# Optimization experiments

Measured on AMD Instinct MI355X. Metric: run time of the kernel, lower is better.

The kernel has to match this reference:

```python
import jax, jax.numpy as jnp
import numpy as np

E = 1024   # embedding_size
K = 64     # key_size
DH = 64    # head_size
H = 16     # layer_size (num heads)
F = 4096   # hidden_size
B, S = 4, 2048
EPS = float(np.finfo(np.float32).eps)  # torch RMSNorm default eps


def setup_inputs() -> dict:
    key = jax.random.key(0)
    ks = jax.random.split(key, 12)
    embeddings = jax.random.normal(ks[0], (B, S, E), dtype=jnp.float32)
    # causal additive mask: 0 on/below diagonal, -1e9 above
    tri = jnp.triu(jnp.ones((S, S), dtype=bool), k=1)
    causal_buffer = jnp.where(tri, -1e9, 0.0).astype(jnp.float32)[None]  # [1,S,S]
    # standard RoPE cos/sin buffers over the key dim
    inv_freq = 1.0 / (10000.0 ** (jnp.arange(0, K // 2, dtype=jnp.float32) * 2.0 / K))
    ang = jnp.arange(S, dtype=jnp.float32)[:, None] * inv_freq[None, :]  # [S,K/2]
    ang = jnp.concatenate([ang, ang], axis=-1)                           # [S,K]
    cos_buffer = jnp.cos(ang)[None]  # [1,S,K]
    sin_buffer = jnp.sin(ang)[None]
    sc = 0.02
    wq = jax.random.normal(ks[1], (H, E, K), dtype=jnp.float32) * sc
    wk = jax.random.normal(ks[2], (H, E, K), dtype=jnp.float32) * sc
    wv = jax.random.normal(ks[3], (H, E, DH), dtype=jnp.float32) * sc
    w_proj = jax.random.normal(ks[4], (E, E), dtype=jnp.float32) * sc
    attn_norm_w = jnp.ones((E,), dtype=jnp.float32)
    mlp_norm_w = jnp.ones((E,), dtype=jnp.float32)
    w_up = jax.random.normal(ks[5], (E, F), dtype=jnp.float32) * sc
    w_gate = jax.random.normal(ks[6], (E, F), dtype=jnp.float32) * sc
    w_down = jax.random.normal(ks[7], (F, E), dtype=jnp.float32) * sc
    return {"embeddings": embeddings, "causal_buffer": causal_buffer,
            "cos_buffer": cos_buffer, "sin_buffer": sin_buffer,
            "wq": wq, "wk": wk, "wv": wv, "w_proj": w_proj,
            "attn_norm_w": attn_norm_w, "mlp_norm_w": mlp_norm_w,
            "w_up": w_up, "w_gate": w_gate, "w_down": w_down}


def _rmsnorm(x, w):
    ms = jnp.mean(x * x, axis=-1, keepdims=True)
    return x * jax.lax.rsqrt(ms + EPS) * w


def _rotate(x, cos, sin):
    # x: [B,H,S,K]; cos/sin: [1,1,S,K]. swapped = cat(second_half, first_half)
    swapped = jnp.concatenate([x[..., K // 2:], x[..., :K // 2]], axis=-1)
    return cos * x + sin * swapped


def reference(embeddings, causal_buffer, cos_buffer, sin_buffer,
              wq, wk, wv, w_proj, attn_norm_w, mlp_norm_w,
              w_up, w_gate, w_down):
    cos = cos_buffer[:, None]  # [1,1,S,K]
    sin = sin_buffer[:, None]
    # NOTE: original computes attention_norm(embeddings) but feeds RAW
    # embeddings to the heads; we reproduce that faithfully.
    q = _rotate(jnp.einsum('bse,hek->bhsk', embeddings, wq), cos, sin)
    k = _rotate(jnp.einsum('bse,hek->bhsk', embeddings, wk), cos, sin)
    v = jnp.einsum('bse,hed->bhsd', embeddings, wv)
    scores = jnp.einsum('bhsk,bhtk->bhst', q, k) / jnp.sqrt(jnp.float32(K))
    scores = scores + causal_buffer[:, None]  # broadcast over heads
    weights = jax.nn.softmax(scores, axis=-1)
    attn = jnp.einsum('bhst,bhtd->bhsd', weights, v)  # [B,H,S,DH]
    attn = attn.transpose(0, 2, 1, 3).reshape(attn.shape[0], attn.shape[2], H * DH)
    x = embeddings + attn @ w_proj
    h = _rmsnorm(x, mlp_norm_w)
    mlp = (h @ w_up) * jax.nn.elu(h @ w_gate)
    return x + mlp @ w_down
```

## Files before the change

kernel.cpp:

```cpp
#include <hip/hip_runtime.h>
#include <cstdint>
#include <cstddef>

#define E_DIM 1024
#define S_LEN 2048
#define NB 4
#define NH 16
#define F_DIM 4096

typedef __attribute__((ext_vector_type(8))) __bf16 bf16x8;
typedef __attribute__((ext_vector_type(4))) __bf16 bf16x4;
typedef __attribute__((ext_vector_type(4))) float f32x4;
typedef __attribute__((ext_vector_type(16))) float f32x16;

__device__ __forceinline__ f32x4 mfma16(bf16x8 a, bf16x8 b, f32x4 c) {
  return __builtin_amdgcn_mfma_f32_16x16x32_bf16(a, b, c, 0, 0, 0);
}
__device__ __forceinline__ f32x16 mfma32(bf16x8 a, bf16x8 b, f32x16 c) {
  return __builtin_amdgcn_mfma_f32_32x32x16_bf16(a, b, c, 0, 0, 0);
}

__device__ __forceinline__ unsigned short f2bf(float f) {
  __bf16 h = (__bf16)f;
  return __builtin_bit_cast(unsigned short, h);
}

__device__ __forceinline__ void gl_lds16(const void* gptr, void* lptr) {
  __builtin_amdgcn_global_load_lds(
      (const __attribute__((address_space(1))) void*)gptr,
      (__attribute__((address_space(3))) void*)lptr, 16, 0, 0);
}


__global__ __launch_bounds__(256) void cast_emb_kernel(
    const float4* __restrict__ in, ushort4* __restrict__ out) {
  int i = blockIdx.x * 256 + threadIdx.x;
  float4 v = in[i];
  ushort4 o;
  o.x = f2bf(v.x); o.y = f2bf(v.y); o.z = f2bf(v.z); o.w = f2bf(v.w);
  out[i] = o;
}

__global__ __launch_bounds__(256) void transpose_cast_kernel(
    const float* __restrict__ in, unsigned short* __restrict__ out, int R, int C) {
  __shared__ float tile[32][33];
  const int bz = blockIdx.z;
  const float* ip = in + (size_t)bz * R * C;
  const int r0 = blockIdx.y * 32, c0 = blockIdx.x * 32;
  const int tc = threadIdx.x & 31, tr = threadIdx.x >> 5;
#pragma unroll
  for (int i = 0; i < 4; ++i)
    tile[tr + i * 8][tc] = ip[(size_t)(r0 + tr + i * 8) * C + (c0 + tc)];
  __syncthreads();
#pragma unroll
  for (int i = 0; i < 4; ++i)
    out[(size_t)(bz * C + c0 + tr + i * 8) * R + (r0 + tc)] = f2bf(tile[tc][tr + i * 8]);
}

__global__ __launch_bounds__(256) void transpose_cast_qkv(
    const float* __restrict__ wq, const float* __restrict__ wk,
    const float* __restrict__ wv, unsigned short* __restrict__ out) {
  __shared__ float tile[32][33];
  const int bz = blockIdx.z;
  const int which = bz >> 4, hz = bz & 15;
  const float* ip =
      (which == 0 ? wq : which == 1 ? wk : wv) + (size_t)hz * 1024 * 64;
  unsigned short* op = out + (size_t)which * 1024 * 1024;
  const int r0 = blockIdx.y * 32, c0 = blockIdx.x * 32;
  const int tc = threadIdx.x & 31, tr = threadIdx.x >> 5;
#pragma unroll
  for (int i = 0; i < 4; ++i)
    tile[tr + i * 8][tc] = ip[(size_t)(r0 + tr + i * 8) * 64 + (c0 + tc)];
  __syncthreads();
#pragma unroll
  for (int i = 0; i < 4; ++i)
    op[(size_t)(hz * 64 + c0 + tr + i * 8) * 1024 + (r0 + tc)] =
        f2bf(tile[tc][tr + i * 8]);
}

__global__ __launch_bounds__(256) void transpose_cast_upgate(
    const float* __restrict__ wup, const float* __restrict__ wgate,
    unsigned short* __restrict__ out) {
  __shared__ float tile[32][33];
  const int z = blockIdx.z & 1;
  const float* ip = z ? wgate : wup;
  const int r0 = blockIdx.y * 32, c0 = blockIdx.x * 32;
  const int tc = threadIdx.x & 31, tr = threadIdx.x >> 5;
#pragma unroll
  for (int i = 0; i < 4; ++i)
    tile[tr + i * 8][tc] = ip[(size_t)(r0 + tr + i * 8) * F_DIM + (c0 + tc)];
  __syncthreads();
#pragma unroll
  for (int i = 0; i < 4; ++i) {
    const int c = c0 + tr + i * 8;
    const int row = 64 * (c >> 5) + (c & 31) + z * 32;
    out[(size_t)row * E_DIM + (r0 + tc)] = f2bf(tile[tc][tr + i * 8]);
  }
}

template <int EPI, int KD>
__global__ __launch_bounds__(256) void gemm_bt(
    const unsigned short* __restrict__ A, const unsigned short* __restrict__ Bt,
    const float* __restrict__ aux, const float* __restrict__ cosb,
    const float* __restrict__ sinb,
    unsigned short* __restrict__ qout, unsigned short* __restrict__ kout,
    unsigned short* __restrict__ vtout, float* __restrict__ fout,
    unsigned short* __restrict__ gout) {
  __shared__ unsigned short As[128 * 64];
  __shared__ unsigned short Bs[128 * 64];
  const int t = threadIdx.x;
  const int lane = t & 63, w = t >> 6;
  const int l31 = lane & 31, half = lane >> 5;
  const int wm = (w >> 1) * 64, wn = (w & 1) * 64;
  const int m0 = blockIdx.y * 128, n0 = blockIdx.x * 128;
  const int sr = t >> 3, sc = t & 7;
  const int gcoff = (sc ^ (sr & 7)) * 8;
  const unsigned short* ga = A + (size_t)(m0 + sr) * KD + gcoff;
  const unsigned short* gb = Bt + (size_t)(n0 + sr) * KD + gcoff;
  unsigned short* lA = &As[sr * 64 + sc * 8];
  unsigned short* lB = &Bs[sr * 64 + sc * 8];
  const int xh = lane & 7;
  f32x16 acc[2][2] = {};
  for (int k0 = 0; k0 < KD; k0 += 64) {
    __syncthreads();
#pragma unroll
    for (int i = 0; i < 4; ++i) {
      gl_lds16(ga + (size_t)(i * 32) * KD + k0, lA + i * 32 * 64);
      gl_lds16(gb + (size_t)(i * 32) * KD + k0, lB + i * 32 * 64);
    }
    __syncthreads();
#pragma unroll
    for (int ksl = 0; ksl < 4; ++ksl) {
      const int cp = ((ksl * 2 + half) ^ xh) * 8;
      bf16x8 af[2], bfr[2];
#pragma unroll
      for (int mi = 0; mi < 2; ++mi)
        af[mi] = *reinterpret_cast<const bf16x8*>(&As[(wm + mi * 32 + l31) * 64 + cp]);
#pragma unroll
      for (int ni = 0; ni < 2; ++ni)
        bfr[ni] = *reinterpret_cast<const bf16x8*>(&Bs[(wn + ni * 32 + l31) * 64 + cp]);
#pragma unroll
      for (int mi = 0; mi < 2; ++mi)
#pragma unroll
        for (int ni = 0; ni < 2; ++ni)
          acc[mi][ni] = mfma32(af[mi], bfr[ni], acc[mi][ni]);
    }
  }
  if (EPI == 0) {
#pragma unroll
    for (int mi = 0; mi < 2; ++mi)
#pragma unroll
      for (int ni = 0; ni < 2; ++ni) {
        const int n = n0 + wn + ni * 32 + l31;
        const int seg = n >> 10, rest = n & 1023, hh = rest >> 6, kk = rest & 63;
#pragma unroll
        for (int reg = 0; reg < 16; ++reg) {
          const int m = m0 + wm + mi * 32 + (reg & 3) + 8 * (reg >> 2) + 4 * half;
          const int b = m >> 11, s = m & 2047;
          const float v = acc[mi][ni][reg];
          if (seg == 2) {
            vtout[(((size_t)(b * NH + hh)) * 64 + kk) * S_LEN + s] = f2bf(v);
          } else {
            const float sw = acc[mi][ni ^ 1][reg];
            const float cv = cosb[s * 64 + kk], sv = sinb[s * 64 + kk];
            const float scl = (seg == 0) ? 0.125f : 1.0f;
            unsigned short* dst = (seg == 0) ? qout : kout;
            dst[(((size_t)(b * NH + hh)) * S_LEN + s) * 64 + kk] =
                f2bf((cv * v + sv * sw) * scl);
          }
        }
      }
  } else {
#pragma unroll
    for (int mi = 0; mi < 2; ++mi)
#pragma unroll
      for (int ni = 0; ni < 2; ++ni) {
        const int n = n0 + wn + ni * 32 + l31;
#pragma unroll
        for (int reg = 0; reg < 16; ++reg) {
          const int m = m0 + wm + mi * 32 + (reg & 3) + 8 * (reg >> 2) + 4 * half;
          const size_t idx = (size_t)m * 1024 + n;
          fout[idx] = aux[idx] + acc[mi][ni][reg];
        }
      }
  }
}

#define FENCE() asm volatile("" ::: "memory")
#define BARX()                        \
  do {                                \
    FENCE();                          \
    __builtin_amdgcn_s_barrier();     \
    FENCE();                          \
  } while (0)

__global__ __launch_bounds__(512, 2) void gemm256_upgate(
    const unsigned short* __restrict__ A, const unsigned short* __restrict__ Bt,
    unsigned short* __restrict__ gout) {
  constexpr int KD = 1024;
  constexpr int NT = KD / 64;
  __shared__ unsigned short L[8 * 8192];
  const int tid = threadIdx.x;
  const int lane = tid & 63, w = tid >> 6;
  const int l31 = lane & 31, half = lane >> 5;
  const int wm = (w >> 2) * 128, wn = (w & 3) * 64;
  const int m0 = blockIdx.y * 256, n0 = blockIdx.x * 256;
  const int r = tid >> 2;
  const int csrc = ((tid & 3) ^ ((r ^ (r >> 2)) & 3)) * 8;
  const unsigned short* gA = A + (size_t)(m0 + r) * KD + csrc;
  const unsigned short* gB = Bt + (size_t)(n0 + r) * KD + csrc;
  const int ldst = tid * 8;
  const int sA = (l31 ^ (l31 >> 2)) & 3;

  f32x16 acc[4][2] = {};
  bf16x8 a[4], b[2];

#define STG(ridx, gp, koff)                                                    \
  do {                                                                         \
    gl_lds16((gp) + (koff), &L[(ridx) * 8192 + ldst]);                         \
    gl_lds16((gp) + (koff) + (size_t)128 * KD,                                 \
             &L[(ridx) * 8192 + 4096 + ldst]);                                 \
  } while (0)

#define RD(hh, kl, bufi)                                                       \
  do {                                                                         \
    const int xo = ((((kl) * 2 + half) ^ sA)) * 8;                             \
    const int ra = ((bufi) * 4 + 1 + 2 * (hh)) * 8192;                         \
    const int rb = ((bufi) * 4 + 2 * (hh)) * 8192;                             \
    _Pragma("unroll") for (int mi = 0; mi < 4; ++mi)                           \
        a[mi] = *reinterpret_cast<const bf16x8*>(                              \
            &L[ra + (wm + mi * 32 + l31) * 32 + xo]);                          \
    _Pragma("unroll") for (int ni = 0; ni < 2; ++ni)                           \
        b[ni] = *reinterpret_cast<const bf16x8*>(                              \
            &L[rb + (wn + ni * 32 + l31) * 32 + xo]);                          \
  } while (0)

#define MFMA8()                                                                \
  do {                                                                         \
    __builtin_amdgcn_s_setprio(1);                                             \
    _Pragma("unroll") for (int mi = 0; mi < 4; ++mi)                           \
        _Pragma("unroll") for (int ni = 0; ni < 2; ++ni)                       \
            acc[mi][ni] = mfma32(a[mi], b[ni], acc[mi][ni]);                   \
    __builtin_amdgcn_s_setprio(0);                                             \
  } while (0)

  STG(0, gB, 0); FENCE();
  STG(1, gA, 0); FENCE();
  STG(2, gB, 32); FENCE();
  STG(3, gA, 32); FENCE();

  int buf = 0;
  for (int t = 0; t < NT; ++t, buf ^= 1) {
    const int nx = buf ^ 1;
    const bool pre = (t + 1 < NT);
    const int ko = (t + 1) * 64;
    asm volatile("s_waitcnt vmcnt(4)" ::: "memory");
    BARX();
    RD(0, 0, buf);
    if (pre) STG(nx * 4 + 0, gB, ko);
    MFMA8();
    BARX();
    RD(0, 1, buf);
    if (pre) STG(nx * 4 + 1, gA, ko);
    MFMA8();
    if (pre) {
      asm volatile("s_waitcnt vmcnt(4)" ::: "memory");
    } else {
      asm volatile("s_waitcnt vmcnt(0)" ::: "memory");
    }
    BARX();
    RD(1, 0, buf);
    if (pre) STG(nx * 4 + 2, gB, ko + 32);
    MFMA8();
    BARX();
    RD(1, 1, buf);
    if (pre) STG(nx * 4 + 3, gA, ko + 32);
    MFMA8();
  }
  const int colb = ((n0 + wn) >> 1) + l31;
#pragma unroll
  for (int mi = 0; mi < 4; ++mi)
#pragma unroll
    for (int reg = 0; reg < 16; ++reg) {
      const int m = m0 + wm + mi * 32 + (reg & 3) + 8 * (reg >> 2) + 4 * half;
      const float uu = acc[mi][0][reg], gg = acc[mi][1][reg];
      const float e = gg > 0.f ? gg : (__expf(gg) - 1.f);
      gout[(size_t)m * F_DIM + colb] = f2bf(uu * e);
    }
#undef STG
#undef RD
#undef MFMA8
}

#define PS_STRIDE 68
__global__ __launch_bounds__(256) void flash_attn(
    const unsigned short* __restrict__ qb, const unsigned short* __restrict__ kb,
    const unsigned short* __restrict__ vtb, unsigned short* __restrict__ attn) {
  __shared__ unsigned short Ks[64 * 64];
  __shared__ unsigned short Vts[64 * 64];
  __shared__ unsigned short Ps[128 * PS_STRIDE];
  const int t = threadIdx.x, lane = t & 63, w = t >> 6;
  const int quad = lane >> 4, l15 = lane & 15;
  const int qt = 15 - blockIdx.y;
  const int bh = blockIdx.x;
  const int b = bh >> 4, hh = bh & 15;
  const unsigned short* qg = qb + (size_t)bh * S_LEN * 64;
  const unsigned short* kg = kb + (size_t)bh * S_LEN * 64;
  const unsigned short* vg = vtb + (size_t)bh * 64 * S_LEN;
  bf16x8 aq[2][2];
#pragma unroll
  for (int mi = 0; mi < 2; ++mi)
#pragma unroll
    for (int ks = 0; ks < 2; ++ks)
      aq[mi][ks] = *reinterpret_cast<const bf16x8*>(
          qg + (size_t)(qt * 128 + w * 32 + mi * 16 + l15) * 64 + ks * 32 + quad * 8);
  f32x4 o[2][4] = {};
  float lpart[2][4] = {};
  const int srk = t >> 3, sck = t & 7;
  const int gck = ((sck ^ (srk & 7)) * 8);
  const int xh = l15 & 7;
  const int ktmax = 2 * qt + 1;
  for (int kt = 0; kt <= ktmax; ++kt) {
    __syncthreads();
#pragma unroll
    for (int i = 0; i < 2; ++i) {
      gl_lds16(kg + (size_t)(kt * 64 + srk + i * 32) * 64 + gck,
               &Ks[(srk + i * 32) * 64 + sck * 8]);
      gl_lds16(vg + (size_t)(srk + i * 32) * S_LEN + kt * 64 + gck,
               &Vts[(srk + i * 32) * 64 + sck * 8]);
    }
    __syncthreads();
    f32x4 sacc[2][4];
#pragma unroll
    for (int mi = 0; mi < 2; ++mi)
#pragma unroll
      for (int nt = 0; nt < 4; ++nt) sacc[mi][nt] = (f32x4){-8.f, -8.f, -8.f, -8.f};
#pragma unroll
    for (int nt = 0; nt < 4; ++nt) {
      bf16x8 b0 = *reinterpret_cast<const bf16x8*>(
          &Ks[(nt * 16 + l15) * 64 + ((quad ^ xh) * 8)]);
      bf16x8 b1 = *reinterpret_cast<const bf16x8*>(
          &Ks[(nt * 16 + l15) * 64 + (((4 + quad) ^ xh) * 8)]);
#pragma unroll
      for (int mi = 0; mi < 2; ++mi) {
        sacc[mi][nt] = mfma16(aq[mi][0], b0, sacc[mi][nt]);
        sacc[mi][nt] = mfma16(aq[mi][1], b1, sacc[mi][nt]);
      }
    }
    if (kt >= 2 * qt) {
#pragma unroll
      for (int mi = 0; mi < 2; ++mi)
#pragma unroll
        for (int nt = 0; nt < 4; ++nt)
#pragma unroll
          for (int rg = 0; rg < 4; ++rg) {
            const int row = qt * 128 + w * 32 + mi * 16 + quad * 4 + rg;
            const int col = kt * 64 + nt * 16 + l15;
            if (col > row) sacc[mi][nt][rg] = -1e9f;
          }
    }
#pragma unroll
    for (int mi = 0; mi < 2; ++mi)
#pragma unroll
      for (int nt = 0; nt < 4; ++nt)
#pragma unroll
        for (int rg = 0; rg < 4; ++rg) {
          const float p = __expf(sacc[mi][nt][rg]);
          lpart[mi][rg] += p;
          Ps[(w * 32 + mi * 16 + quad * 4 + rg) * PS_STRIDE + nt * 16 + l15] = f2bf(p);
        }
#pragma unroll
    for (int ks = 0; ks < 2; ++ks) {
      bf16x8 ap[2];
#pragma unroll
      for (int mi = 0; mi < 2; ++mi) {
        const unsigned short* pp =
            &Ps[(w * 32 + mi * 16 + l15) * PS_STRIDE + ks * 32 + quad * 8];
        bf16x4 lo = *reinterpret_cast<const bf16x4*>(pp);
        bf16x4 hi = *reinterpret_cast<const bf16x4*>(pp + 4);
        ap[mi] = __builtin_shufflevector(lo, hi, 0, 1, 2, 3, 4, 5, 6, 7);
      }
#pragma unroll
      for (int vt = 0; vt < 4; ++vt) {
        bf16x8 bv = *reinterpret_cast<const bf16x8*>(
            &Vts[(vt * 16 + l15) * 64 + (((ks * 4 + quad) ^ xh) * 8)]);
#pragma unroll
        for (int mi = 0; mi < 2; ++mi) o[mi][vt] = mfma16(ap[mi], bv, o[mi][vt]);
      }
    }
  }
  float linv[2][4];
#pragma unroll
  for (int mi = 0; mi < 2; ++mi)
#pragma unroll
    for (int rg = 0; rg < 4; ++rg) {
      float rs = lpart[mi][rg];
#pragma unroll
      for (int d = 1; d < 16; d <<= 1) rs += __shfl_xor(rs, d);
      linv[mi][rg] = 1.0f / rs;
    }
#pragma unroll
  for (int mi = 0; mi < 2; ++mi)
#pragma unroll
    for (int vt = 0; vt < 4; ++vt)
#pragma unroll
      for (int rg = 0; rg < 4; ++rg) {
        const int row = w * 32 + mi * 16 + quad * 4 + rg;
        const int s = qt * 128 + row;
        const float ov = o[mi][vt][rg] * linv[mi][rg];
        attn[((size_t)(b * S_LEN + s)) * E_DIM + hh * 64 + vt * 16 + l15] = f2bf(ov);
      }
}

__global__ __launch_bounds__(256) void rmsnorm_kernel(
    const float* __restrict__ x, const float* __restrict__ wgt,
    unsigned short* __restrict__ hout) {
  const int row = blockIdx.x;
  const int t = threadIdx.x;
  const float4 v = reinterpret_cast<const float4*>(x + (size_t)row * E_DIM)[t];
  float ss = v.x * v.x + v.y * v.y + v.z * v.z + v.w * v.w;
#pragma unroll
  for (int d = 1; d < 64; d <<= 1) ss += __shfl_xor(ss, d);
  __shared__ float red[4];
  if ((t & 63) == 0) red[t >> 6] = ss;
  __syncthreads();
  const float tot = red[0] + red[1] + red[2] + red[3];
  const float sc = rsqrtf(tot * (1.f / 1024.f) + 1.1920929e-07f);
  const float4 g = reinterpret_cast<const float4*>(wgt)[t];
  ushort4 ov;
  ov.x = f2bf(v.x * sc * g.x);
  ov.y = f2bf(v.y * sc * g.y);
  ov.z = f2bf(v.z * sc * g.z);
  ov.w = f2bf(v.w * sc * g.w);
  reinterpret_cast<ushort4*>(hout + (size_t)row * E_DIM)[t] = ov;
}

extern "C" void kernel_launch(void* const* d_in, const int* in_sizes, int n_in,
                              void* d_out, int out_size, void* d_ws, size_t ws_size,
                              hipStream_t stream) {
  (void)in_sizes; (void)n_in; (void)out_size; (void)ws_size;
  const float* emb = (const float*)d_in[0];
  const float* cosb = (const float*)d_in[2];
  const float* sinb = (const float*)d_in[3];
  const float* wq = (const float*)d_in[4];
  const float* wk = (const float*)d_in[5];
  const float* wv = (const float*)d_in[6];
  const float* wproj = (const float*)d_in[7];
  const float* mlpw = (const float*)d_in[9];
  const float* wup = (const float*)d_in[10];
  const float* wgate = (const float*)d_in[11];
  const float* wdown = (const float*)d_in[12];
  float* out = (float*)d_out;
  char* ws = (char*)d_ws;
  unsigned short* wqkv_t = (unsigned short*)(ws + 0);
  unsigned short* wproj_t = (unsigned short*)(ws + 6291456);
  unsigned short* wupgate_t = (unsigned short*)(ws + 8388608);
  unsigned short* wdown_t = (unsigned short*)(ws + 25165824);
  unsigned short* embb = (unsigned short*)(ws + 33554432);
  unsigned short* qbuf = (unsigned short*)(ws + 50331648);
  unsigned short* kbuf = (unsigned short*)(ws + 67108864);
  unsigned short* vtbuf = (unsigned short*)(ws + 83886080);
  unsigned short* gbuf = (unsigned short*)(ws + 33554432);
  unsigned short* attnb = (unsigned short*)(ws + 100663296);
  float* xbuf = (float*)(ws + 117440512);
  unsigned short* hbuf = (unsigned short*)(ws + 150994944);

  dim3 blk(256);
  cast_emb_kernel<<<8192, blk, 0, stream>>>((const float4*)emb, (ushort4*)embb);
  transpose_cast_qkv<<<dim3(2, 32, 48), blk, 0, stream>>>(wq, wk, wv, wqkv_t);
  transpose_cast_kernel<<<dim3(32, 32, 1), blk, 0, stream>>>(wproj, wproj_t, 1024, 1024);
  transpose_cast_upgate<<<dim3(128, 32, 2), blk, 0, stream>>>(wup, wgate, wupgate_t);
  transpose_cast_kernel<<<dim3(32, 128, 1), blk, 0, stream>>>(wdown, wdown_t, 4096, 1024);
  gemm_bt<0, 1024><<<dim3(24, 64), blk, 0, stream>>>(
      embb, wqkv_t, nullptr, cosb, sinb, qbuf, kbuf, vtbuf, nullptr, nullptr);
  flash_attn<<<dim3(64, 16), blk, 0, stream>>>(qbuf, kbuf, vtbuf, attnb);
  gemm_bt<1, 1024><<<dim3(8, 64), blk, 0, stream>>>(
      attnb, wproj_t, emb, nullptr, nullptr, nullptr, nullptr, nullptr, xbuf, nullptr);
  rmsnorm_kernel<<<8192, blk, 0, stream>>>(xbuf, mlpw, hbuf);
  gemm256_upgate<<<dim3(32, 32), dim3(512), 0, stream>>>(hbuf, wupgate_t, gbuf);
  gemm_bt<2, 4096><<<dim3(8, 64), blk, 0, stream>>>(
      gbuf, wdown_t, xbuf, nullptr, nullptr, nullptr, nullptr, nullptr, out, nullptr);
}
```

Baseline: 634.5 us.

## Add dedicated down-projection GEMM with 256x128 tiles and triple-buffered LDS pipeline

Replaces the generic gemm_bt call for the down projection (K=4096) with a specialized kernel. It uses 256x128 block tiles, a three-stage LDS buffer ring fed by direct global-to-LDS loads with explicit vmcnt waits, and a block-index remap so that each XCD works on a contiguous group of M rows for better L2 reuse. The intent is to hide global load latency behind MFMA work and raise arithmetic intensity. In exchange it uses much more LDS (one block per CU) and launches only 256 blocks, which may leave some CUs underused.

```diff
diff --git a/kernel.cpp b/kernel.cpp
--- a/kernel.cpp
+++ b/kernel.cpp
@@ -193,6 +193,8 @@
     __builtin_amdgcn_s_barrier();     \
     FENCE();                          \
   } while (0)
+#define VMW_(n) asm volatile("s_waitcnt vmcnt(" #n ")" ::: "memory")
+#define VMW(n) VMW_(n)
 
 __global__ __launch_bounds__(512, 2) void gemm256_upgate(
     const unsigned short* __restrict__ A, const unsigned short* __restrict__ Bt,
@@ -254,7 +256,7 @@
     const int nx = buf ^ 1;
     const bool pre = (t + 1 < NT);
     const int ko = (t + 1) * 64;
-    asm volatile("s_waitcnt vmcnt(4)" ::: "memory");
+    VMW(4);
     BARX();
     RD(0, 0, buf);
     if (pre) STG(nx * 4 + 0, gB, ko);
@@ -264,9 +266,9 @@
     if (pre) STG(nx * 4 + 1, gA, ko);
     MFMA8();
     if (pre) {
-      asm volatile("s_waitcnt vmcnt(4)" ::: "memory");
+      VMW(4);
     } else {
-      asm volatile("s_waitcnt vmcnt(0)" ::: "memory");
+      VMW(0);
     }
     BARX();
     RD(1, 0, buf);
@@ -290,6 +292,112 @@
 #undef STG
 #undef RD
 #undef MFMA8
+}
+
+__global__ __launch_bounds__(256, 1) void gemm_down(
+    const unsigned short* __restrict__ A, const unsigned short* __restrict__ Bt,
+    const float* __restrict__ aux, float* __restrict__ fout) {
+  constexpr int KD = 4096;
+  constexpr int NT = KD / 64;
+  __shared__ unsigned short L[3 * 24576];
+  const int tid = threadIdx.x;
+  const int lane = tid & 63, w = tid >> 6;
+  const int l31 = lane & 31, half = lane >> 5;
+  const int wm = (w >> 1) * 128, wn = (w & 1) * 64;
+  const int f = blockIdx.y * 8 + blockIdx.x;
+  const int xcd = f & 7, loc = f >> 3;
+  const int m0 = (xcd * 4 + (loc >> 3)) * 256;
+  const int n0 = (loc & 7) * 128;
+  const int r = tid >> 2;
+  const int csrc = ((tid & 3) ^ ((r ^ (r >> 2)) & 3)) * 8;
+  const unsigned short* gA = A + (size_t)(m0 + r) * KD + csrc;
+  const unsigned short* gB = Bt + (size_t)(n0 + r) * KD + csrc;
+  const int ldst = tid * 8;
+  const int sA = (l31 ^ (l31 >> 2)) & 3;
+
+  f32x16 acc[4][2] = {};
+  bf16x8 a[4], b[2];
+
+#define STG_HALF(hh, tt, bufw)                                                 \
+  do {                                                                         \
+    const size_t ko = (size_t)(tt) * 64 + (hh) * 32;                           \
+    unsigned short* Lb = &L[(bufw) * 24576 + (hh) * 12288];                    \
+    gl_lds16(gB + ko, Lb + ldst);                                              \
+    gl_lds16(gB + ko + (size_t)64 * KD, Lb + 2048 + ldst);                     \
+    gl_lds16(gA + ko, Lb + 4096 + ldst);                                       \
+    gl_lds16(gA + ko + (size_t)64 * KD, Lb + 6144 + ldst);                     \
+    gl_lds16(gA + ko + (size_t)128 * KD, Lb + 8192 + ldst);                    \
+    gl_lds16(gA + ko + (size_t)192 * KD, Lb + 10240 + ldst);                   \
+    FENCE();                                                                   \
+  } while (0)
+
+#define RDF(kl, hh, base_)                                                     \
+  do {                                                                         \
+    const int xo = (((kl) * 2 + half) ^ sA) * 8;                               \
+    const unsigned short* Lr = &L[(base_) + (hh) * 12288];                     \
+    _Pragma("unroll") for (int ni = 0; ni < 2; ++ni)                           \
+        b[ni] = *reinterpret_cast<const bf16x8*>(                              \
+            &Lr[(wn + ni * 32 + l31) * 32 + xo]);                              \
+    _Pragma("unroll") for (int mi = 0; mi < 4; ++mi)                           \
+        a[mi] = *reinterpret_cast<const bf16x8*>(                              \
+            &Lr[4096 + (wm + mi * 32 + l31) * 32 + xo]);                       \
+  } while (0)
+
+#define MFMA8D()                                                               \
+  do {                                                                         \
+    __builtin_amdgcn_s_setprio(1);                                             \
+    _Pragma("unroll") for (int mi = 0; mi < 4; ++mi)                           \
+        _Pragma("unroll") for (int ni = 0; ni < 2; ++ni)                       \
+            acc[mi][ni] = mfma32(a[mi], b[ni], acc[mi][ni]);                   \
+    __builtin_amdgcn_s_setprio(0);                                             \
+  } while (0)
+
+#define PHASED(hh, bufr, VM, tt_issue, bufw, DO_ISSUE)                         \
+  do {                                                                         \
+    VMW(VM);                                                                   \
+    BARX();                                                                    \
+    const int base_ = (bufr) * 24576;                                          \
+    RDF(0, hh, base_);                                                         \
+    if (DO_ISSUE) STG_HALF(hh, tt_issue, bufw);                                \
+    MFMA8D();                                                                  \
+    RDF(1, hh, base_);                                                         \
+    MFMA8D();                                                                  \
+  } while (0)
+
+  STG_HALF(0, 0, 0);
+  STG_HALF(1, 0, 0);
+  STG_HALF(0, 1, 1);
+  STG_HALF(1, 1, 1);
+
+  int br = 0;
+  for (int t = 0; t < NT - 2; ++t) {
+    const int bw = (br >= 1) ? br - 1 : br + 2;
+    PHASED(0, br, 18, t + 2, bw, true);
+    PHASED(1, br, 18, t + 2, bw, true);
+    br = (br == 2) ? 0 : br + 1;
+  }
+  PHASED(0, br, 18, 0, 0, false);
+  PHASED(1, br, 12, 0, 0, false);
+  br = (br == 2) ? 0 : br + 1;
+  PHASED(0, br, 6, 0, 0, false);
+  PHASED(1, br, 0, 0, 0, false);
+
+#pragma unroll
+  for (int mi = 0; mi < 4; ++mi)
+#pragma unroll
+    for (int ni = 0; ni < 2; ++ni) {
+      const int n = n0 + wn + ni * 32 + l31;
+#pragma unroll
+      for (int reg = 0; reg < 16; ++reg) {
+        const int m = m0 + wm + mi * 32 + (reg & 3) + 8 * (reg >> 2) + 4 * half;
+        const size_t idx = (size_t)m * 1024 + n;
+        fout[idx] = aux[idx] + acc[mi][ni][reg];
+      }
+    }
+#undef STG_HALF
+#undef RDF
+#undef MFMA8D
+#undef PHASED
 }
 
 #define PS_STRIDE 68
@@ -478,6 +586,5 @@
       attnb, wproj_t, emb, nullptr, nullptr, nullptr, nullptr, nullptr, xbuf, nullptr);
   rmsnorm_kernel<<<8192, blk, 0, stream>>>(xbuf, mlpw, hbuf);
   gemm256_upgate<<<dim3(32, 32), dim3(512), 0, stream>>>(hbuf, wupgate_t, gbuf);
-  gemm_bt<2, 4096><<<dim3(8, 64), blk, 0, stream>>>(
-      gbuf, wdown_t, xbuf, nullptr, nullptr, nullptr, nullptr, nullptr, out, nullptr);
-}
+  gemm_down<<<dim3(8, 32), blk, 0, stream>>>(gbuf, wdown_t, xbuf, out);
+}
```

New measurement: 594.9 us. 1.07x faster.
